# Optimization experiments

Hardware: AMD Instinct MI355X
Metric: run time of the kernel (lower is better)

The kernel has to match this reference:

```python
import jax, jax.numpy as jnp
import numpy as np

HEADS = 6
EPS = 1e-5

def conv1x1(x, w):
    return jax.lax.conv_general_dilated(x, w, (1, 1), 'VALID',
        dimension_numbers=('NCHW', 'OIHW', 'NCHW'))

def dwconv3x3(x, w):
    # depthwise 3x3, padding 1; w: [C,1,3,3]
    return jax.lax.conv_general_dilated(x, w, (1, 1), ((1, 1), (1, 1)),
        dimension_numbers=('NCHW', 'OIHW', 'NCHW'), feature_group_count=x.shape[1])

def layernorm(x, w, b):
    # WithBias LayerNorm over channel dim (applied per pixel)
    mu = x.mean(axis=1, keepdims=True)
    var = ((x - mu) ** 2).mean(axis=1, keepdims=True)
    return (x - mu) * jax.lax.rsqrt(var + EPS) * w[None, :, None, None] + b[None, :, None, None]

def l2norm(t):
    # matches torch F.normalize(dim=-1): norm clamped at 1e-12
    n = jnp.sqrt(jnp.sum(t * t, axis=-1, keepdims=True))
    return t / jnp.maximum(n, 1e-12)

def attention(x, f, qkv_w, dw_w, proj_w, temp):
    xin = x + f
    b, c, h, w = xin.shape
    qkv = dwconv3x3(conv1x1(xin, qkv_w), dw_w)
    q, k, v = jnp.split(qkv, 3, axis=1)
    hd = c // HEADS
    q = l2norm(q.reshape(b, HEADS, hd, h * w))
    k = l2norm(k.reshape(b, HEADS, hd, h * w))
    v = v.reshape(b, HEADS, hd, h * w)
    attn = jnp.einsum('bhcn,bhdn->bhcd', q, k) * temp[None]  # [b,H,hd,hd]
    attn = jax.nn.softmax(attn, axis=-1)
    out = jnp.einsum('bhcd,bhdn->bhcn', attn, v).reshape(b, c, h, w)
    return conv1x1(out, proj_w)

def ffn(x, in_w, dw_w, out_w):
    x = conv1x1(x, in_w)
    x1, x2 = jnp.split(dwconv3x3(x, dw_w), 2, axis=1)
    return conv1x1(jax.nn.gelu(x1, approximate=False) * x2, out_w)

def setup_inputs() -> dict:
    key = jax.random.key(0)
    B, C, H, W = 2, 96, 256, 256
    HID = int(C * 2.66)  # 255
    ks = jax.random.split(key, 32)
    p = lambda k, shp: (0.02 * jax.random.normal(k, shp, dtype=jnp.float32))
    d = {
        'Fw': jax.random.normal(ks[0], (B, C, H, W), dtype=jnp.float32),
        'F0_c': jax.random.normal(ks[1], (B, C, H, W), dtype=jnp.float32),
        'Kd': jax.random.normal(ks[2], (B, C, H, W), dtype=jnp.float32),
        'ln1_w': jnp.ones((C,), jnp.float32), 'ln1_b': jnp.zeros((C,), jnp.float32),
        'a1_qkv_w': p(ks[3], (3 * C, C, 1, 1)), 'a1_dw_w': p(ks[4], (3 * C, 1, 3, 3)),
        'a1_proj_w': p(ks[5], (C, C, 1, 1)), 'a1_temp': jnp.ones((HEADS, 1, 1), jnp.float32),
        'ln2_w': jnp.ones((C,), jnp.float32), 'ln2_b': jnp.zeros((C,), jnp.float32),
        'f1_in_w': p(ks[6], (2 * HID, C, 1, 1)), 'f1_dw_w': p(ks[7], (2 * HID, 1, 3, 3)),
        'f1_out_w': p(ks[8], (C, HID, 1, 1)),
        'ln3_w': jnp.ones((C,), jnp.float32), 'ln3_b': jnp.zeros((C,), jnp.float32),
        'a2_qkv_w': p(ks[9], (3 * C, C, 1, 1)), 'a2_dw_w': p(ks[10], (3 * C, 1, 3, 3)),
        'a2_proj_w': p(ks[11], (C, C, 1, 1)), 'a2_temp': jnp.ones((HEADS, 1, 1), jnp.float32),
        'ln4_w': jnp.ones((C,), jnp.float32), 'ln4_b': jnp.zeros((C,), jnp.float32),
        'f2_in_w': p(ks[12], (2 * HID, C, 1, 1)), 'f2_dw_w': p(ks[13], (2 * HID, 1, 3, 3)),
        'f2_out_w': p(ks[14], (C, HID, 1, 1)),
    }
    return d

def reference(Fw, F0_c, Kd, ln1_w, ln1_b, a1_qkv_w, a1_dw_w, a1_proj_w, a1_temp,
              ln2_w, ln2_b, f1_in_w, f1_dw_w, f1_out_w,
              ln3_w, ln3_b, a2_qkv_w, a2_dw_w, a2_proj_w, a2_temp,
              ln4_w, ln4_b, f2_in_w, f2_dw_w, f2_out_w):
    x = Fw + attention(layernorm(Fw, ln1_w, ln1_b), F0_c, a1_qkv_w, a1_dw_w, a1_proj_w, a1_temp)
    x = x + ffn(layernorm(x, ln2_w, ln2_b), f1_in_w, f1_dw_w, f1_out_w)
    x = x + attention(layernorm(x, ln3_w, ln3_b), Kd, a2_qkv_w, a2_dw_w, a2_proj_w, a2_temp)
    x = x + ffn(layernorm(x, ln4_w, ln4_b), f2_in_w, f2_dw_w, f2_out_w)
    return x
```

## Files before the change

### kernel.cpp

```cpp
#include <hip/hip_runtime.h>
#include <math.h>

using u16 = unsigned short;
using u32 = unsigned int;
typedef __attribute__((ext_vector_type(8))) short bf16x8;
typedef __attribute__((ext_vector_type(4))) float f32x4;
typedef __attribute__((ext_vector_type(16))) float f32x16;

#define NPLANE 65536
#define BELEMS ((size_t)6291456)
#define ASTR   ((size_t)33423360)
#define BSTR   ((size_t)18874368)

__device__ __forceinline__ float bf2f(u16 u) { return __uint_as_float(((u32)u) << 16); }
__device__ __forceinline__ u16 f2bf(float f) {
  if (!__builtin_isfinite(f)) return (u16)0x5F80;
  u32 u = __float_as_uint(f);
  return (u16)((u + 0x7fffu + ((u >> 16) & 1u)) >> 16);
}
__device__ __forceinline__ float4 cvt4(ushort4 v) {
  return make_float4(bf2f(v.x), bf2f(v.y), bf2f(v.z), bf2f(v.w));
}

union U16x8 { uint4 u4; bf16x8 v; u16 s[8]; };

__global__ void k_detect(const u16* __restrict__ p, u32* __restrict__ flag) {
  if (blockIdx.x == 0 && threadIdx.x == 0) *flag = (p[0] == (u16)0x3F80) ? 0u : 1u;
}

__device__ __forceinline__ float ldf(const void* p, int i, bool f32) {
  return f32 ? ((const float*)p)[i] : bf2f(((const u16*)p)[i]);
}

__global__ __launch_bounds__(256) void k_cvt_all(
    const void* p0, const void* p1, const void* p2, const void* p3,
    const void* p4, const void* p5, const void* p6, const void* p7,
    const void* p8, const void* p9, const void* p10, const void* p11,
    const void* p12, const void* p13, const void* p14, const void* p15,
    float* __restrict__ dst, const u32* __restrict__ fl)
{
  const int i = blockIdx.x * 256 + threadIdx.x;
  if (i >= 33576) return;
  const bool xf = (*fl != 0);
  const void* s; int o;
  if      (i < 2592)  { s = p0;  o = i; }
  else if (i < 7182)  { s = p1;  o = i - 2592; }
  else if (i < 9774)  { s = p2;  o = i - 7182; }
  else if (i < 14364) { s = p3;  o = i - 9774; }
  else if (i < 23580) { s = p4;  o = i - 14364; }
  else if (i < 32796) { s = p5;  o = i - 23580; }
  else if (i < 32802) { s = p6;  o = i - 32796; }
  else if (i < 32808) { s = p7;  o = i - 32802; }
  else if (i < 32904) { s = p8;  o = i - 32808; }
  else if (i < 33000) { s = p9;  o = i - 32904; }
  else if (i < 33096) { s = p10; o = i - 33000; }
  else if (i < 33192) { s = p11; o = i - 33096; }
  else if (i < 33288) { s = p12; o = i - 33192; }
  else if (i < 33384) { s = p13; o = i - 33288; }
  else if (i < 33480) { s = p14; o = i - 33384; }
  else                { s = p15; o = i - 33480; }
  dst[i] = ldf(s, o, xf);
}

__global__ __launch_bounds__(256) void k_wprep_all(
    const void* q1, const void* i1, const void* o1,
    const void* q2, const void* i2, const void* o2,
    u16* __restrict__ wbuf, const u32* __restrict__ fl)
{
  const int idx = blockIdx.x * 256 + threadIdx.x;
  if (idx >= 215040) return;
  const bool xf = (*fl != 0);
  const void* s; int local, M, Kr, Kpad;
  if      (idx < 27648)  { s = q1; local = idx;          M = 288; Kr = 96;  Kpad = 96;  }
  else if (idx < 82944)  { s = i1; local = idx - 27648;  M = 510; Kr = 96;  Kpad = 96;  }
  else if (idx < 107520) { s = o1; local = idx - 82944;  M = 96;  Kr = 255; Kpad = 256; }
  else if (idx < 135168) { s = q2; local = idx - 107520; M = 288; Kr = 96;  Kpad = 96;  }
  else if (idx < 190464) { s = i2; local = idx - 135168; M = 510; Kr = 96;  Kpad = 96;  }
  else                   { s = o2; local = idx - 190464; M = 96;  Kr = 255; Kpad = 256; }
  const int m = local / Kpad, k = local - m * Kpad;
  u16 v = 0;
  if (m < M && k < Kr) v = f2bf(ldf(s, m * Kr + k, xf));
  wbuf[idx] = v;
}

__global__ __launch_bounds__(256) void k_lnp(
    const void* __restrict__ x, const u32* __restrict__ xfl,
    const void* __restrict__ f, const u32* __restrict__ ffl,
    const float* __restrict__ lnw, const float* __restrict__ lnb,
    u16* __restrict__ xT)
{
  __shared__ float xin[96 * 64];
  __shared__ float fin[96 * 64];
  __shared__ float ps[256], pq[256];
  __shared__ float mu[64], rsd[64];
  const int tid = threadIdx.x;
  const int pix0 = blockIdx.x * 64;
  const int z = blockIdx.z;
  const size_t eb = (size_t)z * BELEMS;
  u16* xTo = xT + (size_t)z * BSTR;
  const bool xf = xfl && (*xfl != 0);
  const bool ff = ffl && (*ffl != 0);

#pragma unroll
  for (int i = 0; i < 6; ++i) {
    const int u = tid + i * 256;
    const int c = u >> 4, p4 = (u & 15) << 2;
    const size_t base = eb + (size_t)c * NPLANE + pix0 + p4;
    const float4 v = xf ? *(const float4*)((const float*)x + base)
                        : cvt4(*(const ushort4*)((const u16*)x + base));
    *(float4*)(xin + c * 64 + p4) = v;
    if (f) {
      const float4 fv = ff ? *(const float4*)((const float*)f + base)
                           : cvt4(*(const ushort4*)((const u16*)f + base));
      *(float4*)(fin + c * 64 + p4) = fv;
    }
  }
  __syncthreads();
  {
    const int p = tid & 63, qq = tid >> 6;
    float s = 0.f, q = 0.f;
    const int c0 = qq * 24;
#pragma unroll 8
    for (int c = c0; c < c0 + 24; ++c) {
      const float v = xin[c * 64 + p];
      s += v; q += v * v;
    }
    ps[tid] = s; pq[tid] = q;
  }
  __syncthreads();
  if (tid < 64) {
    const float s = ps[tid] + ps[tid + 64] + ps[tid + 128] + ps[tid + 192];
    const float q = pq[tid] + pq[tid + 64] + pq[tid + 128] + pq[tid + 192];
    const float m = s * (1.f / 96.f);
    mu[tid] = m;
    rsd[tid] = rsqrtf(fmaxf(q * (1.f / 96.f) - m * m, 0.f) + 1e-5f);
  }
  __syncthreads();
#pragma unroll
  for (int i = 0; i < 6; ++i) {
    const int u = tid + i * 256;
    const int c = u >> 4, p4 = (u & 15) << 2;
    const float4 v = *(const float4*)(xin + c * 64 + p4);
    const float w = lnw[c], b = lnb[c];
    float o0 = (v.x - mu[p4 + 0]) * rsd[p4 + 0] * w + b;
    float o1 = (v.y - mu[p4 + 1]) * rsd[p4 + 1] * w + b;
    float o2 = (v.z - mu[p4 + 2]) * rsd[p4 + 2] * w + b;
    float o3 = (v.w - mu[p4 + 3]) * rsd[p4 + 3] * w + b;
    if (f) {
      const float4 fv = *(const float4*)(fin + c * 64 + p4);
      o0 += fv.x; o1 += fv.y; o2 += fv.z; o3 += fv.w;
    }
    *(float4*)(xin + c * 64 + p4) = make_float4(o0, o1, o2, o3);
  }
  __syncthreads();
#pragma unroll
  for (int i = 0; i < 3; ++i) {
    const int u = tid + i * 256;
    const int px = u / 12, q = u - px * 12;
    U16x8 pk;
#pragma unroll
    for (int e = 0; e < 8; ++e) pk.s[e] = f2bf(xin[(q * 8 + e) * 64 + px]);
    *(uint4*)(xTo + (size_t)(pix0 + px) * 96 + q * 8) = pk.u4;
  }
}

__global__ __launch_bounds__(256) void k_tr(
    const u16* __restrict__ in, u16* __restrict__ outT, int K, int Kpad)
{
  __shared__ u16 tile[64][72];
  const int n0 = blockIdx.x * 64;
  const int k0 = blockIdx.y * 64;
  const int z = blockIdx.z;
  const u16* inp = in + (size_t)z * BSTR;
  u16* op0 = outT + (size_t)z * ASTR;
  const int t = threadIdx.x;
#pragma unroll
  for (int j = 0; j < 2; ++j) {
    const int idx = t + j * 256;
    const int kr = idx >> 3, q = idx & 7;
    const int k = k0 + kr;
    uint4 v = make_uint4(0u, 0u, 0u, 0u);
    if (k < K) v = *(const uint4*)(inp + (size_t)k * NPLANE + n0 + q * 8);
    *(uint4*)(&tile[kr][q * 8]) = v;
  }
  __syncthreads();
  const int px = t & 63, kq = t >> 6;
  const int kbase = k0 + kq * 16;
  if (kbase < Kpad) {
    u16* op = op0 + (size_t)(n0 + px) * Kpad + kbase;
#pragma unroll
    for (int kk = 0; kk < 16; kk += 8) {
      U16x8 pk;
#pragma unroll
      for (int e = 0; e < 8; ++e) pk.s[e] = tile[kq * 16 + kk + e][px];
      *(uint4*)(op + kk) = pk.u4;
    }
  }
}

__global__ __launch_bounds__(256) void k_gemm_bt(
    const u16* __restrict__ BT, size_t bts, const u16* __restrict__ A, int ats,
    int Kpad, int OC,
    const void* __restrict__ res, const u32* __restrict__ rfl,
    void* __restrict__ out, const u32* __restrict__ ofl, size_t ots)
{
  __shared__ u16 Bs[128 * 136];
  const int t = threadIdx.x;
  const int oc0 = blockIdx.x * 96;
  const int n0 = blockIdx.y * 128;
  const int z = blockIdx.z;
  const u16* BTz = BT + (size_t)z * bts;
  const u16* Az = A + (size_t)z * (size_t)ats;
  const size_t ob = (size_t)z * ots;
  const size_t rb = (size_t)z * BELEMS;
  const int l = t & 63, wid = t >> 6, wm = wid >> 1, wn = wid & 1;

  f32x4 acc[3][4];
#pragma unroll
  for (int m = 0; m < 3; ++m)
#pragma unroll
    for (int n = 0; n < 4; ++n) acc[m][n] = (f32x4){0.f, 0.f, 0.f, 0.f};

  for (int kb = 0; kb < Kpad; kb += 128) {
    const int kc = min(128, Kpad - kb);
    const int LP = kc + 8;
    const int nu4 = kc >> 3;
    if (kb) __syncthreads();
    for (int u = t; u < 128 * nu4; u += 256) {
      const int r = u / nu4, q = u - r * nu4;
      *(uint4*)(Bs + r * LP + q * 8) = *(const uint4*)(BTz + (size_t)(n0 + r) * Kpad + kb + q * 8);
    }
    __syncthreads();
    const int nks = kc >> 5;
    for (int ks = 0; ks < nks; ++ks) {
      const int kk = (ks << 5) + ((l >> 4) << 3);
      U16x8 a[3], b[4];
#pragma unroll
      for (int m = 0; m < 3; ++m)
        a[m].u4 = *(const uint4*)(Az + (size_t)(oc0 + wm * 48 + m * 16 + (l & 15)) * Kpad + kb + kk);
#pragma unroll
      for (int ns = 0; ns < 4; ++ns)
        b[ns].u4 = *(const uint4*)(Bs + (wn * 64 + ns * 16 + (l & 15)) * LP + kk);
#pragma unroll
      for (int m = 0; m < 3; ++m)
#pragma unroll
        for (int ns = 0; ns < 4; ++ns)
          acc[m][ns] = __builtin_amdgcn_mfma_f32_16x16x32_bf16(a[m].v, b[ns].v, acc[m][ns], 0, 0, 0);
    }
  }

  const bool rf = rfl && (*rfl != 0);
  const bool of = ofl && (*ofl != 0);
#pragma unroll
  for (int m = 0; m < 3; ++m) {
    const int ocb = oc0 + wm * 48 + m * 16 + ((l >> 4) << 2);
#pragma unroll
    for (int ns = 0; ns < 4; ++ns) {
      const int n = n0 + wn * 64 + ns * 16 + (l & 15);
#pragma unroll
      for (int r = 0; r < 4; ++r) {
        const int oc = ocb + r;
        if (oc < OC) {
          float v = acc[m][ns][r];
          const size_t pi = (size_t)oc * NPLANE + n;
          if (res) v += rf ? ((const float*)res)[rb + pi] : bf2f(((const u16*)res)[rb + pi]);
          if (of) ((float*)out)[ob + pi] = v;
          else    ((u16*)out)[ob + pi] = f2bf(v);
        }
      }
    }
  }
}

__global__ __launch_bounds__(256) void k_dw(
    const u16* __restrict__ in, const float* __restrict__ w9, u16* __restrict__ out)
{
  const int c = blockIdx.y;
  const int r0 = blockIdx.x * 16;
  const int z = blockIdx.z;
  __shared__ float tt[18 * 256];
  const int tid = threadIdx.x;
  const u16* ip = in + (size_t)z * ASTR + (size_t)c * NPLANE;
  for (int u = tid; u < 1152; u += 256) {
    const int r = u >> 6, p4 = (u & 63) << 2;
    const int gr = r0 - 1 + r;
    float4 fv = make_float4(0.f, 0.f, 0.f, 0.f);
    if (gr >= 0 && gr < 256) fv = cvt4(*(const ushort4*)(ip + gr * 256 + p4));
    *(float4*)(tt + r * 256 + p4) = fv;
  }
  float wr[9];
#pragma unroll
  for (int i = 0; i < 9; ++i) wr[i] = w9[c * 9 + i];
  __syncthreads();
  const int col = tid;
  const bool cm = col > 0, cp = col < 255;
  float a0 = cm ? tt[col - 1] : 0.f, a1 = tt[col], a2 = cp ? tt[col + 1] : 0.f;
  float b0 = cm ? tt[256 + col - 1] : 0.f, b1 = tt[256 + col], b2 = cp ? tt[256 + col + 1] : 0.f;
  u16* op = out + (size_t)z * BSTR + (size_t)c * NPLANE + (size_t)r0 * 256 + col;
#pragma unroll
  for (int rr = 0; rr < 16; ++rr) {
    const int rn = (rr + 2) * 256;
    const float c1 = tt[rn + col];
    const float c0 = cm ? tt[rn + col - 1] : 0.f;
    const float c2 = cp ? tt[rn + col + 1] : 0.f;
    const float s = wr[0] * a0 + wr[1] * a1 + wr[2] * a2
                  + wr[3] * b0 + wr[4] * b1 + wr[5] * b2
                  + wr[6] * c0 + wr[7] * c1 + wr[8] * c2;
    op[rr * 256] = f2bf(s);
    a0 = b0; a1 = b1; a2 = b2; b0 = c0; b1 = c1; b2 = c2;
  }
}

__global__ __launch_bounds__(256) void k_dw_gelu(
    const u16* __restrict__ in, const float* __restrict__ w9, u16* __restrict__ out)
{
  const int c = blockIdx.y;
  const int r0 = blockIdx.x * 16;
  const int z = blockIdx.z;
  __shared__ float t1[18 * 256];
  __shared__ float t2[18 * 256];
  const int tid = threadIdx.x;
  const u16* ip1 = in + (size_t)z * ASTR + (size_t)c * NPLANE;
  const u16* ip2 = in + (size_t)z * ASTR + (size_t)(c + 255) * NPLANE;
  for (int u = tid; u < 1152; u += 256) {
    const int r = u >> 6, p4 = (u & 63) << 2;
    const int gr = r0 - 1 + r;
    float4 fa = make_float4(0.f, 0.f, 0.f, 0.f), fb = fa;
    if (gr >= 0 && gr < 256) {
      fa = cvt4(*(const ushort4*)(ip1 + gr * 256 + p4));
      fb = cvt4(*(const ushort4*)(ip2 + gr * 256 + p4));
    }
    *(float4*)(t1 + r * 256 + p4) = fa;
    *(float4*)(t2 + r * 256 + p4) = fb;
  }
  float wa[9], wb9[9];
#pragma unroll
  for (int i = 0; i < 9; ++i) { wa[i] = w9[c * 9 + i]; wb9[i] = w9[(c + 255) * 9 + i]; }
  __syncthreads();
  const int col = tid;
  const bool cm = col > 0, cp = col < 255;
  float a0 = cm ? t1[col - 1] : 0.f, a1 = t1[col], a2 = cp ? t1[col + 1] : 0.f;
  float b0 = cm ? t1[256 + col - 1] : 0.f, b1 = t1[256 + col], b2 = cp ? t1[256 + col + 1] : 0.f;
  float d0 = cm ? t2[col - 1] : 0.f, d1 = t2[col], d2 = cp ? t2[col + 1] : 0.f;
  float e0 = cm ? t2[256 + col - 1] : 0.f, e1 = t2[256 + col], e2 = cp ? t2[256 + col + 1] : 0.f;
  u16* op = out + (size_t)z * BSTR + (size_t)c * NPLANE + (size_t)r0 * 256 + col;
#pragma unroll
  for (int rr = 0; rr < 16; ++rr) {
    const int rn = (rr + 2) * 256;
    const float c1 = t1[rn + col];
    const float c0 = cm ? t1[rn + col - 1] : 0.f;
    const float c2 = cp ? t1[rn + col + 1] : 0.f;
    const float g1 = wa[0] * a0 + wa[1] * a1 + wa[2] * a2
                   + wa[3] * b0 + wa[4] * b1 + wa[5] * b2
                   + wa[6] * c0 + wa[7] * c1 + wa[8] * c2;
    const float f1 = t2[rn + col];
    const float f0 = cm ? t2[rn + col - 1] : 0.f;
    const float f2 = cp ? t2[rn + col + 1] : 0.f;
    const float g2 = wb9[0] * d0 + wb9[1] * d1 + wb9[2] * d2
                   + wb9[3] * e0 + wb9[4] * e1 + wb9[5] * e2
                   + wb9[6] * f0 + wb9[7] * f1 + wb9[8] * f2;
    const float gel = 0.5f * g1 * (1.f + erff(g1 * 0.70710678118654752f));
    op[rr * 256] = f2bf(gel * g2);
    a0 = b0; a1 = b1; a2 = b2; b0 = c0; b1 = c1; b2 = c2;
    d0 = e0; d1 = e1; d2 = e2; e0 = f0; e1 = f1; e2 = f2;
  }
}

__global__ __launch_bounds__(256) void k_reduce_s(
    const u16* __restrict__ qkv, float* __restrict__ S,
    float* __restrict__ qn2, float* __restrict__ kn2)
{
  const int h = blockIdx.y;
  const int n0 = blockIdx.x * 512;
  const int zb = blockIdx.z;
  const u16* qz = qkv + (size_t)zb * BSTR;
  float* Sz = S + zb * 1728;
  float* qn2z = qn2 + zb * 1728;
  float* kn2z = kn2 + zb * 1728;
  __shared__ uint4 st[64 * 33];
  const int tid = threadIdx.x;
  const int l = tid & 63, w = tid >> 6;

#pragma unroll
  for (int i = 0; i < 8; ++i) {
    const int idx = tid + i * 256;
    const int c = idx & 63, r = idx >> 6;
    const int plane = (r < 16) ? (h * 16 + r) : (96 + h * 16 + (r - 16));
    st[c * 33 + r] = *(const uint4*)(qz + (size_t)plane * NPLANE + n0 + c * 8);
  }
  __syncthreads();

  f32x16 acc;
#pragma unroll
  for (int j = 0; j < 16; ++j) acc[j] = 0.f;
  const int row = l & 31;
  const int cg = (w << 4) + (l >> 5);
#pragma unroll
  for (int s = 0; s < 8; ++s) {
    U16x8 frag;
    frag.u4 = st[(cg + s * 2) * 33 + row];
    acc = __builtin_amdgcn_mfma_f32_32x32x16_bf16(frag.v, frag.v, acc, 0, 0, 0);
  }
  __syncthreads();

  float* fs = (float*)st;
#pragma unroll
  for (int j = 0; j < 16; ++j) {
    const int rj = (j & 3) + 8 * (j >> 2) + 4 * (l >> 5);
    fs[w * 1024 + rj * 32 + (l & 31)] = acc[j];
  }
  __syncthreads();
#pragma unroll
  for (int e4 = 0; e4 < 4; ++e4) {
    const int e = tid * 4 + e4;
    const float v = fs[e] + fs[1024 + e] + fs[2048 + e] + fs[3072 + e];
    const int r = e >> 5, cc = e & 31;
    if (r < 16 && cc >= 16) atomicAdd(Sz + h * 256 + r * 16 + (cc - 16), v);
    if (r == cc) {
      if (r < 16) atomicAdd(qn2z + h * 16 + r, v);
      else        atomicAdd(kn2z + h * 16 + (r - 16), v);
    }
  }
}

__global__ __launch_bounds__(256) void k_softmax_m(
    const float* __restrict__ S, const float* __restrict__ qn2, const float* __restrict__ kn2,
    const float* __restrict__ temp, const float* __restrict__ proj, u16* __restrict__ Mtb)
{
  __shared__ float attn[6 * 256];
  const int tid = threadIdx.x;
  const int zb = blockIdx.z;
  const float* Sz = S + zb * 1728;
  const float* qn2z = qn2 + zb * 1728;
  const float* kn2z = kn2 + zb * 1728;
  u16* Mz = Mtb + zb * 9216;
  if (tid < 96) {
    const int h = tid >> 4, i = tid & 15;
    const float qn = fmaxf(sqrtf(qn2z[tid]), 1e-12f);
    const float tp = temp[h];
    float row[16];
    float mx = -3.4e38f;
#pragma unroll
    for (int d = 0; d < 16; ++d) {
      const float kn = fmaxf(sqrtf(kn2z[h * 16 + d]), 1e-12f);
      row[d] = Sz[h * 256 + i * 16 + d] / (qn * kn) * tp;
      mx = fmaxf(mx, row[d]);
    }
    float sum = 0.f;
#pragma unroll
    for (int d = 0; d < 16; ++d) { row[d] = expf(row[d] - mx); sum += row[d]; }
    const float inv = 1.f / sum;
#pragma unroll
    for (int d = 0; d < 16; ++d) attn[h * 256 + i * 16 + d] = row[d] * inv;
  }
  __syncthreads();
  for (int u = tid; u < 9216; u += 256) {
    const int e = u / 96, dg = u - e * 96;
    const int h = dg >> 4, d = dg & 15;
    float s = 0.f;
#pragma unroll
    for (int i = 0; i < 16; ++i)
      s += proj[e * 96 + h * 16 + i] * attn[h * 256 + i * 16 + d];
    Mz[u] = f2bf(s);
  }
}

extern "C" void kernel_launch(void* const* d_in, const int* in_sizes, int n_in,
                              void* d_out, int out_size, void* d_ws, size_t ws_size,
                              hipStream_t stream)
{
  (void)in_sizes; (void)n_in; (void)out_size;
  if (ws_size < (size_t)234975000) return;

  const void* Fw  = d_in[0];
  const void* F0c = d_in[1];
  const void* Kdi = d_in[2];

  char* ws = (char*)d_ws;
  u16* xcur = (u16*)ws;
  u16* bufA = (u16*)(ws + 25165824);
  u16* bufB = (u16*)(ws + 158859264);
  u16* wb   = (u16*)(ws + 234356736);
  u16* Wq1 = wb;           u16* Wi1 = wb + 27648;   u16* Wo1 = wb + 82944;
  u16* Wq2 = wb + 107520;  u16* Wi2 = wb + 135168;  u16* Wo2 = wb + 190464;
  u16* Mtb = wb + 215040;
  float* fz = (float*)(ws + 234823680);
  float* dwA1 = fz;          float* dwF1 = fz + 2592;
  float* dwA2 = fz + 7182;   float* dwF2 = fz + 9774;
  float* prj1 = fz + 14364;  float* prj2 = fz + 23580;
  float* tmp1 = fz + 32796;  float* tmp2 = fz + 32802;
  float* lnp  = fz + 32808;
  float* Sb   = fz + 33576;
  float* Qn   = Sb + 1536;
  float* Kn   = Sb + 1632;
  u32*  flag  = (u32*)(fz + 37032);

  k_detect<<<1, 64, 0, stream>>>((const u16*)d_in[3], flag);

  k_wprep_all<<<dim3(840), 256, 0, stream>>>(d_in[5], d_in[11], d_in[13],
                                             d_in[16], d_in[22], d_in[24], wb, flag);
  k_cvt_all<<<dim3(132), 256, 0, stream>>>(
      d_in[6], d_in[12], d_in[17], d_in[23], d_in[7], d_in[18], d_in[8], d_in[19],
      d_in[3], d_in[4], d_in[9], d_in[10], d_in[14], d_in[15], d_in[20], d_in[21],
      fz, flag);

  auto attn_stage = [&](const void* x, const u32* xfl, const void* f, const u32* ffl,
                        const float* lw, const float* lb, const u16* Wq,
                        const float* dwf, const float* tmpf, const float* prjf,
                        const void* res, const u32* rfl,
                        void* outx, const u32* ofl) {
    hipMemsetAsync(Sb, 0, 2 * 1728 * sizeof(float), stream);
    k_lnp<<<dim3(1024, 1, 2), 256, 0, stream>>>(x, xfl, f, ffl, lw, lb, bufB);
    k_gemm_bt<<<dim3(3, 512, 2), 256, 0, stream>>>(bufB, BSTR, Wq, 0, 96, 288,
                                                   nullptr, nullptr, bufA, nullptr, ASTR);
    k_dw<<<dim3(16, 288, 2), 256, 0, stream>>>(bufA, dwf, bufB);
    k_reduce_s<<<dim3(128, 6, 2), 256, 0, stream>>>(bufB, Sb, Qn, Kn);
    k_softmax_m<<<dim3(1, 1, 2), 256, 0, stream>>>(Sb, Qn, Kn, tmpf, prjf, Mtb);
    k_tr<<<dim3(1024, 2, 2), 256, 0, stream>>>(bufB + (size_t)192 * NPLANE, bufA, 96, 96);
    k_gemm_bt<<<dim3(1, 512, 2), 256, 0, stream>>>(bufA, ASTR, Mtb, 9216, 96, 96,
                                                   res, rfl, outx, ofl, BELEMS);
  };
  auto ffn_stage = [&](const void* x, const u32* xfl,
                       const float* lw, const float* lb, const u16* Wi,
                       const float* dwf, const u16* Wo,
                       void* outx, const u32* ofl) {
    k_lnp<<<dim3(1024, 1, 2), 256, 0, stream>>>(x, xfl, nullptr, nullptr, lw, lb, bufB);
    k_gemm_bt<<<dim3(6, 512, 2), 256, 0, stream>>>(bufB, BSTR, Wi, 0, 96, 510,
                                                   nullptr, nullptr, bufA, nullptr, ASTR);
    k_dw_gelu<<<dim3(16, 255, 2), 256, 0, stream>>>(bufA, dwf, bufB);
    k_tr<<<dim3(1024, 4, 2), 256, 0, stream>>>(bufB, bufA, 255, 256);
    k_gemm_bt<<<dim3(1, 512, 2), 256, 0, stream>>>(bufA, ASTR, Wo, 0, 256, 96,
                                                   x, xfl, outx, ofl, BELEMS);
  };

  attn_stage(Fw, flag, F0c, flag, lnp + 0, lnp + 96, Wq1, dwA1, tmp1, prj1,
             Fw, flag, xcur, nullptr);
  ffn_stage(xcur, nullptr, lnp + 192, lnp + 288, Wi1, dwF1, Wo1, xcur, nullptr);
  attn_stage(xcur, nullptr, Kdi, flag, lnp + 384, lnp + 480, Wq2, dwA2, tmp2, prj2,
             xcur, nullptr, xcur, nullptr);
  ffn_stage(xcur, nullptr, lnp + 576, lnp + 672, Wi2, dwF2, Wo2, d_out, flag);
}
```

Before: 895.5 us.

## Fuse transpose into output-projection GEMMs and stage first-GEMM output through LDS

Drops the separate k_tr transpose kernel. A new k_gemm kernel reads the channel-major activation planes directly and transposes them into XOR-swizzled shared memory while loading its B tile. The input-projection GEMM is specialised for K=96: it loads the whole B tile once, then stages its bf16 results through LDS so the global stores are coalesced 16-byte rows. This removes two launches and a full write and re-read of the intermediate per stage, at the cost of strided 2-byte global gathers inside the GEMM.

```diff
diff --git a/kernel.cpp b/kernel.cpp
--- a/kernel.cpp
+++ b/kernel.cpp
@@ -164,83 +164,131 @@
   }
 }
 
-__global__ __launch_bounds__(256) void k_tr(
-    const u16* __restrict__ in, u16* __restrict__ outT, int K, int Kpad)
-{
-  __shared__ u16 tile[64][72];
-  const int n0 = blockIdx.x * 64;
-  const int k0 = blockIdx.y * 64;
-  const int z = blockIdx.z;
-  const u16* inp = in + (size_t)z * BSTR;
-  u16* op0 = outT + (size_t)z * ASTR;
-  const int t = threadIdx.x;
-#pragma unroll
-  for (int j = 0; j < 2; ++j) {
-    const int idx = t + j * 256;
-    const int kr = idx >> 3, q = idx & 7;
-    const int k = k0 + kr;
-    uint4 v = make_uint4(0u, 0u, 0u, 0u);
-    if (k < K) v = *(const uint4*)(inp + (size_t)k * NPLANE + n0 + q * 8);
-    *(uint4*)(&tile[kr][q * 8]) = v;
-  }
-  __syncthreads();
-  const int px = t & 63, kq = t >> 6;
-  const int kbase = k0 + kq * 16;
-  if (kbase < Kpad) {
-    u16* op = op0 + (size_t)(n0 + px) * Kpad + kbase;
-#pragma unroll
-    for (int kk = 0; kk < 16; kk += 8) {
-      U16x8 pk;
-#pragma unroll
-      for (int e = 0; e < 8; ++e) pk.s[e] = tile[kq * 16 + kk + e][px];
-      *(uint4*)(op + kk) = pk.u4;
-    }
-  }
-}
-
 __global__ __launch_bounds__(256) void k_gemm_bt(
-    const u16* __restrict__ BT, size_t bts, const u16* __restrict__ A, int ats,
-    int Kpad, int OC,
-    const void* __restrict__ res, const u32* __restrict__ rfl,
-    void* __restrict__ out, const u32* __restrict__ ofl, size_t ots)
-{
-  __shared__ u16 Bs[128 * 136];
+    const u16* __restrict__ BT, size_t bts, const u16* __restrict__ A,
+    int OC, u16* __restrict__ out, size_t ots)
+{
+  __shared__ u16 Bs[128 * 104];
   const int t = threadIdx.x;
   const int oc0 = blockIdx.x * 96;
   const int n0 = blockIdx.y * 128;
   const int z = blockIdx.z;
   const u16* BTz = BT + (size_t)z * bts;
-  const u16* Az = A + (size_t)z * (size_t)ats;
-  const size_t ob = (size_t)z * ots;
-  const size_t rb = (size_t)z * BELEMS;
+  u16* outz = out + (size_t)z * ots;
   const int l = t & 63, wid = t >> 6, wm = wid >> 1, wn = wid & 1;
 
+  const uint4* src = (const uint4*)(BTz + (size_t)n0 * 96);
+#pragma unroll
+  for (int i = 0; i < 6; ++i) {
+    const int u = t + i * 256;
+    const int r = u / 12, q = u - r * 12;
+    *(uint4*)(Bs + r * 104 + q * 8) = src[u];
+  }
+  __syncthreads();
+
   f32x4 acc[3][4];
 #pragma unroll
   for (int m = 0; m < 3; ++m)
 #pragma unroll
     for (int n = 0; n < 4; ++n) acc[m][n] = (f32x4){0.f, 0.f, 0.f, 0.f};
 
-  for (int kb = 0; kb < Kpad; kb += 128) {
-    const int kc = min(128, Kpad - kb);
-    const int LP = kc + 8;
-    const int nu4 = kc >> 3;
+#pragma unroll
+  for (int ks = 0; ks < 3; ++ks) {
+    const int kk = (ks << 5) + ((l >> 4) << 3);
+    U16x8 a[3], b[4];
+#pragma unroll
+    for (int m = 0; m < 3; ++m)
+      a[m].u4 = *(const uint4*)(A + (size_t)(oc0 + wm * 48 + m * 16 + (l & 15)) * 96 + kk);
+#pragma unroll
+    for (int ns = 0; ns < 4; ++ns)
+      b[ns].u4 = *(const uint4*)(Bs + (wn * 64 + ns * 16 + (l & 15)) * 104 + kk);
+#pragma unroll
+    for (int m = 0; m < 3; ++m)
+#pragma unroll
+      for (int ns = 0; ns < 4; ++ns)
+        acc[m][ns] = __builtin_amdgcn_mfma_f32_16x16x32_bf16(a[m].v, b[ns].v, acc[m][ns], 0, 0, 0);
+  }
+
+  __syncthreads();
+  u16* ct = Bs;
+#pragma unroll
+  for (int m = 0; m < 3; ++m) {
+    const int rl = wm * 48 + m * 16 + ((l >> 4) << 2);
+#pragma unroll
+    for (int ns = 0; ns < 4; ++ns) {
+      const int nl = wn * 64 + ns * 16 + (l & 15);
+#pragma unroll
+      for (int r = 0; r < 4; ++r) ct[(rl + r) * 136 + nl] = f2bf(acc[m][ns][r]);
+    }
+  }
+  __syncthreads();
+#pragma unroll
+  for (int i = 0; i < 6; ++i) {
+    const int u = t + i * 256;
+    const int r = u >> 4, q = u & 15;
+    if (oc0 + r < OC) {
+      const uint4 pk = *(const uint4*)(ct + r * 136 + q * 8);
+      *(uint4*)(outz + (size_t)(oc0 + r) * NPLANE + n0 + q * 8) = pk;
+    }
+  }
+}
+
+__global__ __launch_bounds__(256) void k_gemm(
+    const u16* __restrict__ xsrc, size_t xzs, const u16* __restrict__ A, int azs,
+    int K, int Kpad, int OC,
+    const void* __restrict__ res, const u32* __restrict__ rfl,
+    void* __restrict__ out, const u32* __restrict__ ofl)
+{
+  __shared__ uint4 Bt[128 * 16];
+  const int t = threadIdx.x;
+  const int p = t & 127, h = t >> 7;
+  const int oc0 = blockIdx.x * 96;
+  const int n0 = blockIdx.y * 128;
+  const int z = blockIdx.z;
+  const u16* xz = xsrc + (size_t)z * xzs;
+  const u16* Az = A + (size_t)z * (size_t)azs;
+  const size_t eb = (size_t)z * BELEMS;
+  const int nglob = n0 + p;
+  const int l = t & 63, wid = t >> 6, wm = wid >> 1, wn = wid & 1;
+
+  f32x4 acc[3][4];
+#pragma unroll
+  for (int m = 0; m < 3; ++m)
+#pragma unroll
+    for (int n = 0; n < 4; ++n) acc[m][n] = (f32x4){0.f, 0.f, 0.f, 0.f};
+
+  for (int kb = 0; kb < K; kb += 128) {
     if (kb) __syncthreads();
-    for (int u = t; u < 128 * nu4; u += 256) {
-      const int r = u / nu4, q = u - r * nu4;
-      *(uint4*)(Bs + r * LP + q * 8) = *(const uint4*)(BTz + (size_t)(n0 + r) * Kpad + kb + q * 8);
+    const int kc = min(128, K - kb);
+    const int U = (kc + 7) >> 3;
+    const int uh = U >> 1;
+    for (int j = 0; j < uh; ++j) {
+      const int u = h * uh + j;
+      const int cb = kb + u * 8;
+      U16x8 pk;
+#pragma unroll
+      for (int e = 0; e < 8; ++e) {
+        const int c = cb + e;
+        pk.s[e] = (c < K) ? xz[(size_t)c * NPLANE + nglob] : (u16)0;
+      }
+      Bt[p * 16 + (u ^ (p & 7))] = pk.u4;
     }
     __syncthreads();
-    const int nks = kc >> 5;
+    const int nks = (kc + 31) >> 5;
     for (int ks = 0; ks < nks; ++ks) {
-      const int kk = (ks << 5) + ((l >> 4) << 3);
       U16x8 a[3], b[4];
-#pragma unroll
-      for (int m = 0; m < 3; ++m)
-        a[m].u4 = *(const uint4*)(Az + (size_t)(oc0 + wm * 48 + m * 16 + (l & 15)) * Kpad + kb + kk);
-#pragma unroll
-      for (int ns = 0; ns < 4; ++ns)
-        b[ns].u4 = *(const uint4*)(Bs + (wn * 64 + ns * 16 + (l & 15)) * LP + kk);
+      const int kk = kb + ks * 32 + ((l >> 4) << 3);
+#pragma unroll
+      for (int m = 0; m < 3; ++m) {
+        const int row = oc0 + wm * 48 + m * 16 + (l & 15);
+        a[m].u4 = ((const uint4*)Az)[((size_t)row * Kpad + kk) >> 3];
+      }
+#pragma unroll
+      for (int ns = 0; ns < 4; ++ns) {
+        const int row = wn * 64 + ns * 16 + (l & 15);
+        const int up = (ks * 4 + (l >> 4)) ^ (row & 7);
+        b[ns].u4 = Bt[row * 16 + up];
+      }
 #pragma unroll
       for (int m = 0; m < 3; ++m)
 #pragma unroll
@@ -262,10 +310,10 @@
         const int oc = ocb + r;
         if (oc < OC) {
           float v = acc[m][ns][r];
-          const size_t pi = (size_t)oc * NPLANE + n;
-          if (res) v += rf ? ((const float*)res)[rb + pi] : bf2f(((const u16*)res)[rb + pi]);
-          if (of) ((float*)out)[ob + pi] = v;
-          else    ((u16*)out)[ob + pi] = f2bf(v);
+          const size_t gi = eb + (size_t)oc * NPLANE + n;
+          if (res) v += rf ? ((const float*)res)[gi] : bf2f(((const u16*)res)[gi]);
+          if (of) ((float*)out)[gi] = v;
+          else    ((u16*)out)[gi] = f2bf(v);
         }
       }
     }
@@ -511,26 +559,23 @@
                         void* outx, const u32* ofl) {
     hipMemsetAsync(Sb, 0, 2 * 1728 * sizeof(float), stream);
     k_lnp<<<dim3(1024, 1, 2), 256, 0, stream>>>(x, xfl, f, ffl, lw, lb, bufB);
-    k_gemm_bt<<<dim3(3, 512, 2), 256, 0, stream>>>(bufB, BSTR, Wq, 0, 96, 288,
-                                                   nullptr, nullptr, bufA, nullptr, ASTR);
+    k_gemm_bt<<<dim3(3, 512, 2), 256, 0, stream>>>(bufB, BSTR, Wq, 288, bufA, ASTR);
     k_dw<<<dim3(16, 288, 2), 256, 0, stream>>>(bufA, dwf, bufB);
     k_reduce_s<<<dim3(128, 6, 2), 256, 0, stream>>>(bufB, Sb, Qn, Kn);
     k_softmax_m<<<dim3(1, 1, 2), 256, 0, stream>>>(Sb, Qn, Kn, tmpf, prjf, Mtb);
-    k_tr<<<dim3(1024, 2, 2), 256, 0, stream>>>(bufB + (size_t)192 * NPLANE, bufA, 96, 96);
-    k_gemm_bt<<<dim3(1, 512, 2), 256, 0, stream>>>(bufA, ASTR, Mtb, 9216, 96, 96,
-                                                   res, rfl, outx, ofl, BELEMS);
+    k_gemm<<<dim3(1, 512, 2), 256, 0, stream>>>(bufB + (size_t)192 * NPLANE, BSTR,
+                                                Mtb, 9216, 96, 96, 96,
+                                                res, rfl, outx, ofl);
   };
   auto ffn_stage = [&](const void* x, const u32* xfl,
                        const float* lw, const float* lb, const u16* Wi,
                        const float* dwf, const u16* Wo,
                        void* outx, const u32* ofl) {
     k_lnp<<<dim3(1024, 1, 2), 256, 0, stream>>>(x, xfl, nullptr, nullptr, lw, lb, bufB);
-    k_gemm_bt<<<dim3(6, 512, 2), 256, 0, stream>>>(bufB, BSTR, Wi, 0, 96, 510,
-                                                   nullptr, nullptr, bufA, nullptr, ASTR);
+    k_gemm_bt<<<dim3(6, 512, 2), 256, 0, stream>>>(bufB, BSTR, Wi, 510, bufA, ASTR);
     k_dw_gelu<<<dim3(16, 255, 2), 256, 0, stream>>>(bufA, dwf, bufB);
-    k_tr<<<dim3(1024, 4, 2), 256, 0, stream>>>(bufB, bufA, 255, 256);
-    k_gemm_bt<<<dim3(1, 512, 2), 256, 0, stream>>>(bufA, ASTR, Wo, 0, 256, 96,
-                                                   x, xfl, outx, ofl, BELEMS);
+    k_gemm<<<dim3(1, 512, 2), 256, 0, stream>>>(bufB, BSTR, Wo, 0, 255, 256, 96,
+                                                x, xfl, outx, ofl);
   };
 
   attn_stage(Fw, flag, F0c, flag, lnp + 0, lnp + 96, Wq1, dwA1, tmp1, prj1,
```

After: 744.0 us. 16.9% less time.
